# Optimization experiments

Hardware: AMD Instinct MI355X
Metric: run time of the kernel (lower is better)

Reference implementation:

```python
import jax, jax.numpy as jnp
import numpy as np

K = 7          # involution kernel size
GC = 16        # group_channels
BN_EPS = 1e-5


def conv1x1(x, w, b):
    # x: [b,c,h,w], w: [o,c], b: [o]
    return jnp.einsum('bchw,oc->bohw', x, w) + b[None, :, None, None]


def involution(x, w1, b1, w2, b2):
    # x: [b,c,h,w]; stride=1, kernel K, padding K//2
    b_, c, h, w = x.shape
    g = c // GC
    # per-pixel kernel weights: conv1x1 -> conv1x1 (no activation, as in source)
    wgt = conv1x1(conv1x1(x, w1, b1), w2, b2).reshape(b_, g, K * K, h, w)
    # patches: [b, c*K*K, h, w] with channel-major (c, kh, kw) ordering, matching torch Unfold
    pat = jax.lax.conv_general_dilated_patches(
        x, (K, K), (1, 1), ((K // 2, K // 2), (K // 2, K // 2)))
    pat = pat.reshape(b_, g, GC, K * K, h, w)
    out = jnp.einsum('bgkhw,bgckhw->bgchw', wgt, pat)
    return out.reshape(b_, c, h, w)


def hswish(x):
    return x * jnp.clip(x + 3.0, 0.0, 6.0) / 6.0


def setup_inputs() -> dict:
    key = jax.random.key(0)
    ks = jax.random.split(key, 20)
    inp, oup, mip = 256, 256, 64
    n, h, w = 16, 96, 96
    rr = 4  # involution reduction_ratio

    def rn(k, shape, s=0.05):
        return (jax.random.normal(k, shape) * s).astype(jnp.float32)

    def invp(k0, k1, k2, k3):
        return (rn(k0, (mip // rr, mip)), rn(k1, (mip // rr,)),
                rn(k2, (K * K * (mip // GC), mip // rr)),
                rn(k3, (K * K * (mip // GC),)))

    d = {}
    d['x'] = jax.random.normal(ks[0], (n, inp, h, w), dtype=jnp.float32)
    d['w_c1'] = rn(ks[1], (mip, inp)); d['b_c1'] = rn(ks[2], (mip,))
    d['inv1_w1'], d['inv1_b1'], d['inv1_w2'], d['inv1_b2'] = invp(ks[3], ks[4], ks[5], ks[6])
    d['bn_g'] = jnp.ones(mip, jnp.float32); d['bn_b'] = jnp.zeros(mip, jnp.float32)
    d['bn_m'] = jnp.zeros(mip, jnp.float32); d['bn_v'] = jnp.ones(mip, jnp.float32)
    d['invh_w1'], d['invh_b1'], d['invh_w2'], d['invh_b2'] = invp(ks[7], ks[8], ks[9], ks[10])
    d['w_h'] = rn(ks[11], (oup, mip)); d['b_h'] = rn(ks[12], (oup,))
    d['invw_w1'], d['invw_b1'], d['invw_w2'], d['invw_b2'] = invp(ks[13], ks[14], ks[15], ks[16])
    d['w_w'] = rn(ks[17], (oup, mip)); d['b_w'] = rn(ks[18], (oup,))
    return d


def reference(x, w_c1, b_c1, inv1_w1, inv1_b1, inv1_w2, inv1_b2,
              bn_g, bn_b, bn_m, bn_v,
              invh_w1, invh_b1, invh_w2, invh_b2, w_h, b_h,
              invw_w1, invw_b1, invw_w2, invw_b2, w_w, b_w):
    n, c, h, w = x.shape
    x_h = jnp.mean(x, axis=3, keepdims=True)                        # [n,c,h,1]
    x_w = jnp.mean(x, axis=2, keepdims=True).transpose(0, 1, 3, 2)  # [n,c,w,1]
    y = jnp.concatenate([x_h, x_w], axis=2)                          # [n,c,h+w,1]
    y = conv1x1(y, w_c1, b_c1)                                       # [n,mip,h+w,1]
    y = involution(y, inv1_w1, inv1_b1, inv1_w2, inv1_b2)
    inv_std = jax.lax.rsqrt(bn_v + BN_EPS)
    y = (y - bn_m[None, :, None, None]) * (bn_g * inv_std)[None, :, None, None] + bn_b[None, :, None, None]
    y = hswish(y)
    y_h = y[:, :, :h, :]                                             # [n,mip,h,1]
    y_w = y[:, :, h:, :].transpose(0, 1, 3, 2)                       # [n,mip,1,w]
    a_h = jax.nn.sigmoid(conv1x1(involution(y_h, invh_w1, invh_b1, invh_w2, invh_b2), w_h, b_h))
    a_w = jax.nn.sigmoid(conv1x1(involution(y_w, invw_w1, invw_b1, invw_w2, invw_b2), w_w, b_w))
    return x * a_w * a_h
```

## Files before the change

### kernel.cpp

```cpp
#include <hip/hip_runtime.h>
#include <math.h>

#define N_B   16
#define C_IN  256
#define MIP   64
#define HW    96
#define PTOT  192
#define KK    7

typedef float floatx4 __attribute__((ext_vector_type(4)));

__global__ void pool_kernel(const float* __restrict__ x, float* __restrict__ pooled) {
    int plane = blockIdx.x;
    const float* xp = x + (size_t)plane * (HW * HW);
    __shared__ float sm[HW * 97];
    int t = threadIdx.x;
    #pragma unroll
    for (int k = 0; k < 9; ++k) {
        int idx = t + k * 256;
        floatx4 v = ((const floatx4*)xp)[idx];
        int flat = idx * 4;
        int row = flat / HW;
        int col = flat - row * HW;
        float* d = &sm[row * 97 + col];
        d[0] = v.x; d[1] = v.y; d[2] = v.z; d[3] = v.w;
    }
    __syncthreads();
    float* pp = pooled + (size_t)plane * PTOT;
    if (t < HW) {
        float rs = 0.f;
        #pragma unroll 4
        for (int j = 0; j < HW; ++j) rs += sm[t * 97 + j];
        pp[t] = rs * (1.f / 96.f);
    } else if (t < 2 * HW) {
        int c = t - HW;
        float cs = 0.f;
        #pragma unroll 4
        for (int i = 0; i < HW; ++i) cs += sm[i * 97 + c];
        pp[HW + c] = cs * (1.f / 96.f);
    }
}

__global__ __launch_bounds__(256) void megamid_kernel(
    const float* __restrict__ pooled,
    const float* __restrict__ w_c1, const float* __restrict__ b_c1,
    const float* __restrict__ i1_w1, const float* __restrict__ i1_b1,
    const float* __restrict__ i1_w2, const float* __restrict__ i1_b2,
    const float* __restrict__ bn_g, const float* __restrict__ bn_b,
    const float* __restrict__ bn_m, const float* __restrict__ bn_v,
    const float* __restrict__ h_w1, const float* __restrict__ h_b1,
    const float* __restrict__ h_w2, const float* __restrict__ h_b2,
    const float* __restrict__ w_h,  const float* __restrict__ b_h,
    const float* __restrict__ v_w1, const float* __restrict__ v_b1,
    const float* __restrict__ v_w2, const float* __restrict__ v_b2,
    const float* __restrict__ w_w,  const float* __restrict__ b_w,
    float* __restrict__ a_h, float* __restrict__ a_w)
{
    int p0 = blockIdx.x * 16;
    int n  = blockIdx.y;
    int t  = threadIdx.x;
    int side = (p0 >= HW) ? 1 : 0;
    int lo = side * HW;

    __shared__ float smem[15552];
    float* pt   = smem;
    float* sw   = smem + 8192;
    float* y0t  = smem + 12352;
    float* yt   = smem + 14144;
    float* lt    = smem;
    float* lwgt  = smem + 352;
    float* lt2   = smem + 968;
    float* lwgt2 = smem + 1224;
    float* lz    = smem + 1672;

    const float* pn = pooled + (size_t)n * C_IN * PTOT;

    #pragma unroll
    for (int i = 0; i < 32; ++i) {
        int flat = t + 256 * i;
        int c = flat >> 5, j = flat & 31;
        int r = p0 - 6 + j;
        pt[flat] = (j < 28 && r >= 0 && r < PTOT) ? pn[c * PTOT + r] : 0.f;
    }

    int o = t & 63;
    int j0 = (t >> 6) * 8;
    float acc[8];
    #pragma unroll
    for (int e = 0; e < 8; ++e) acc[e] = 0.f;

    for (int c0 = 0; c0 < C_IN; c0 += 64) {
        __syncthreads();
        #pragma unroll
        for (int i = 0; i < 16; ++i) {
            int flat = t + 256 * i;
            int oo = flat >> 6, cc = flat & 63;
            sw[oo * 65 + cc] = w_c1[oo * C_IN + c0 + cc];
        }
        __syncthreads();
        #pragma unroll 4
        for (int cc = 0; cc < 64; ++cc) {
            float wv = sw[o * 65 + cc];
            const floatx4 pa = *(const floatx4*)&pt[(c0 + cc) * 32 + j0];
            const floatx4 pb = *(const floatx4*)&pt[(c0 + cc) * 32 + j0 + 4];
            acc[0] += wv * pa.x; acc[1] += wv * pa.y;
            acc[2] += wv * pa.z; acc[3] += wv * pa.w;
            acc[4] += wv * pb.x; acc[5] += wv * pb.y;
            acc[6] += wv * pb.z; acc[7] += wv * pb.w;
        }
    }
    {
        float bo = b_c1[o];
        #pragma unroll
        for (int e = 0; e < 8; ++e) {
            int j = j0 + e;
            if (j < 28) {
                int r = p0 - 6 + j;
                y0t[j * 64 + o] = (r >= 0 && r < PTOT) ? (acc[e] + bo) : 0.f;
            }
        }
    }
    __syncthreads();

    for (int idx = t; idx < 352; idx += 256) {
        int q = idx >> 4, i = idx & 15;
        float a = i1_b1[i];
        const float* wr = i1_w1 + i * MIP;
        #pragma unroll 8
        for (int oo = 0; oo < MIP; ++oo) a += wr[oo] * y0t[(q + 3) * 64 + oo];
        lt[idx] = a;
    }
    __syncthreads();
    for (int idx = t; idx < 616; idx += 256) {
        int q = idx / 28, m = idx - q * 28;
        int g = m / 7, ky = m - g * 7;
        int wq = g * 49 + ky * 7 + 3;
        float a = i1_b2[wq];
        const float* wr = i1_w2 + wq * 16;
        #pragma unroll
        for (int r = 0; r < 16; ++r) a += wr[r] * lt[q * 16 + r];
        lwgt[idx] = a;
    }
    __syncthreads();
    for (int idx = t; idx < 1408; idx += 256) {
        int q = idx >> 6, ch = idx & 63;
        int g = ch >> 4;
        float a = 0.f;
        #pragma unroll
        for (int ky = 0; ky < KK; ++ky)
            a += lwgt[q * 28 + g * 7 + ky] * y0t[(q + ky) * 64 + ch];
        float inv_std = rsqrtf(bn_v[ch] + 1e-5f);
        float v = (a - bn_m[ch]) * (bn_g[ch] * inv_std) + bn_b[ch];
        yt[idx] = v * fminf(fmaxf(v + 3.f, 0.f), 6.f) * (1.f / 6.f);
    }
    __syncthreads();

    const float* ww1 = side ? v_w1 : h_w1;
    const float* bb1 = side ? v_b1 : h_b1;
    const float* ww2 = side ? v_w2 : h_w2;
    const float* bb2 = side ? v_b2 : h_b2;
    const float* wf  = side ? w_w  : w_h;
    const float* bf  = side ? b_w  : b_h;

    {
        int pp = t >> 4, i = t & 15;
        float a = bb1[i];
        const float* wr = ww1 + i * MIP;
        #pragma unroll 8
        for (int oo = 0; oo < MIP; ++oo) a += wr[oo] * yt[(pp + 3) * 64 + oo];
        lt2[t] = a;
    }
    __syncthreads();
    for (int idx = t; idx < 448; idx += 256) {
        int pp = idx / 28, m = idx - pp * 28;
        int g = m / 7, kk = m - g * 7;
        int wq = side ? (g * 49 + 21 + kk) : (g * 49 + kk * 7 + 3);
        float a = bb2[wq];
        const float* wr = ww2 + wq * 16;
        #pragma unroll
        for (int r = 0; r < 16; ++r) a += wr[r] * lt2[pp * 16 + r];
        lwgt2[idx] = a;
    }
    __syncthreads();
    for (int idx = t; idx < 1024; idx += 256) {
        int pp = idx >> 6, ch = idx & 63;
        int g = ch >> 4;
        float a = 0.f;
        #pragma unroll
        for (int k = 0; k < KK; ++k) {
            int pos = p0 + pp + k - 3;
            float v = (pos >= lo && pos < lo + HW) ? yt[(pp + k) * 64 + ch] : 0.f;
            a += lwgt2[pp * 28 + g * 7 + k] * v;
        }
        lz[idx] = a;
    }
    __syncthreads();
    {
        int co = t;
        float accf[16];
        float bfv = bf[co];
        #pragma unroll
        for (int pp = 0; pp < 16; ++pp) accf[pp] = bfv;
        const float* wr = wf + co * MIP;
        for (int ch = 0; ch < MIP; ++ch) {
            float wv = wr[ch];
            #pragma unroll
            for (int pp = 0; pp < 16; ++pp)
                accf[pp] += wv * lz[pp * 64 + ch];
        }
        float* dst = side ? a_w : a_h;
        size_t basep = ((size_t)n * C_IN + co) * HW + (p0 - lo);
        #pragma unroll
        for (int pp = 0; pp < 16; ++pp)
            dst[basep + pp] = 1.f / (1.f + __expf(-accf[pp]));
    }
}

__global__ void apply_kernel(const float* __restrict__ x,
                             const float* __restrict__ a_h, const float* __restrict__ a_w,
                             float* __restrict__ out) {
    int plane = blockIdx.x;
    const floatx4* xp = (const floatx4*)(x + (size_t)plane * (HW * HW));
    floatx4* op = (floatx4*)(out + (size_t)plane * (HW * HW));
    __shared__ float sah[HW];
    __shared__ float saw[HW];
    int t = threadIdx.x;
    if (t < HW) {
        sah[t] = a_h[(size_t)plane * HW + t];
        saw[t] = a_w[(size_t)plane * HW + t];
    }
    __syncthreads();
    #pragma unroll
    for (int k = 0; k < 9; ++k) {
        int idx = t + k * 256;
        floatx4 v = xp[idx];
        int row = idx / 24;
        int c4 = (idx - row * 24) * 4;
        float ah = sah[row];
        v.x *= ah * saw[c4 + 0];
        v.y *= ah * saw[c4 + 1];
        v.z *= ah * saw[c4 + 2];
        v.w *= ah * saw[c4 + 3];
        __builtin_nontemporal_store(v, &op[idx]);
    }
}

extern "C" void kernel_launch(void* const* d_in, const int* in_sizes, int n_in,
                              void* d_out, int out_size, void* d_ws, size_t ws_size,
                              hipStream_t stream) {
    const float* x      = (const float*)d_in[0];
    const float* w_c1   = (const float*)d_in[1];
    const float* b_c1   = (const float*)d_in[2];
    const float* i1_w1  = (const float*)d_in[3];
    const float* i1_b1  = (const float*)d_in[4];
    const float* i1_w2  = (const float*)d_in[5];
    const float* i1_b2  = (const float*)d_in[6];
    const float* bn_g   = (const float*)d_in[7];
    const float* bn_b   = (const float*)d_in[8];
    const float* bn_m   = (const float*)d_in[9];
    const float* bn_v   = (const float*)d_in[10];
    const float* ih_w1  = (const float*)d_in[11];
    const float* ih_b1  = (const float*)d_in[12];
    const float* ih_w2  = (const float*)d_in[13];
    const float* ih_b2  = (const float*)d_in[14];
    const float* w_h    = (const float*)d_in[15];
    const float* b_h    = (const float*)d_in[16];
    const float* iw_w1  = (const float*)d_in[17];
    const float* iw_b1  = (const float*)d_in[18];
    const float* iw_w2  = (const float*)d_in[19];
    const float* iw_b2  = (const float*)d_in[20];
    const float* w_w    = (const float*)d_in[21];
    const float* b_w    = (const float*)d_in[22];
    float* out = (float*)d_out;

    float* ws = (float*)d_ws;
    float* pooled = ws;
    float* a_h    = pooled + 786432;
    float* a_w    = a_h + 393216;

    pool_kernel<<<dim3(N_B * C_IN), dim3(256), 0, stream>>>(x, pooled);
    megamid_kernel<<<dim3(12, N_B), dim3(256), 0, stream>>>(
        pooled, w_c1, b_c1, i1_w1, i1_b1, i1_w2, i1_b2,
        bn_g, bn_b, bn_m, bn_v,
        ih_w1, ih_b1, ih_w2, ih_b2, w_h, b_h,
        iw_w1, iw_b1, iw_w2, iw_b2, w_w, b_w, a_h, a_w);
    apply_kernel<<<dim3(N_B * C_IN), dim3(256), 0, stream>>>(x, a_h, a_w, out);
}
```

Baseline: 353.8 us.

## Split fused mid kernel into conv, involution and final projection kernels

Splits the monolithic per-block pipeline into three kernels: a 1x1 conv over pooled features, the involution/BN/hswish stage with smaller position tiles, and a final projection+sigmoid kernel with many more blocks. The intermediates go through global workspace buffers that alias earlier, already-consumed buffers. The aim is to replace a low-occupancy, 192-block kernel that ran long serial phases with higher parallelism. The cost is extra launches and global round trips for the intermediates.

```diff
diff --git a/kernel.cpp b/kernel.cpp
--- a/kernel.cpp
+++ b/kernel.cpp
@@ -41,97 +41,75 @@
     }
 }
 
-__global__ __launch_bounds__(256) void megamid_kernel(
+__global__ __launch_bounds__(256) void conv_kernel(
     const float* __restrict__ pooled,
     const float* __restrict__ w_c1, const float* __restrict__ b_c1,
+    float* __restrict__ y0g)
+{
+    int t = threadIdx.x;
+    int o  = t & 63;
+    int pl = t >> 6;
+    int p  = blockIdx.x * 4 + pl;
+    int n  = blockIdx.y;
+    const float* pr = pooled + (size_t)n * C_IN * PTOT + p;
+    const floatx4* wr = (const floatx4*)(w_c1 + o * C_IN);
+    float acc = 0.f;
+    #pragma unroll 8
+    for (int c4 = 0; c4 < C_IN / 4; ++c4) {
+        floatx4 w4 = wr[c4];
+        int c = c4 * 4;
+        acc += w4.x * pr[(c + 0) * PTOT];
+        acc += w4.y * pr[(c + 1) * PTOT];
+        acc += w4.z * pr[(c + 2) * PTOT];
+        acc += w4.w * pr[(c + 3) * PTOT];
+    }
+    y0g[((size_t)n * PTOT + p) * 64 + o] = acc + b_c1[o];
+}
+
+__global__ __launch_bounds__(256) void mid_kernel(
+    const float* __restrict__ y0g,
     const float* __restrict__ i1_w1, const float* __restrict__ i1_b1,
     const float* __restrict__ i1_w2, const float* __restrict__ i1_b2,
     const float* __restrict__ bn_g, const float* __restrict__ bn_b,
     const float* __restrict__ bn_m, const float* __restrict__ bn_v,
     const float* __restrict__ h_w1, const float* __restrict__ h_b1,
     const float* __restrict__ h_w2, const float* __restrict__ h_b2,
-    const float* __restrict__ w_h,  const float* __restrict__ b_h,
     const float* __restrict__ v_w1, const float* __restrict__ v_b1,
     const float* __restrict__ v_w2, const float* __restrict__ v_b2,
-    const float* __restrict__ w_w,  const float* __restrict__ b_w,
-    float* __restrict__ a_h, float* __restrict__ a_w)
+    float* __restrict__ lzg)
 {
-    int p0 = blockIdx.x * 16;
+    int p0 = blockIdx.x * 8;
     int n  = blockIdx.y;
     int t  = threadIdx.x;
     int side = (p0 >= HW) ? 1 : 0;
     int lo = side * HW;
 
-    __shared__ float smem[15552];
-    float* pt   = smem;
-    float* sw   = smem + 8192;
-    float* y0t  = smem + 12352;
-    float* yt   = smem + 14144;
-    float* lt    = smem;
-    float* lwgt  = smem + 352;
-    float* lt2   = smem + 968;
-    float* lwgt2 = smem + 1224;
-    float* lz    = smem + 1672;
-
-    const float* pn = pooled + (size_t)n * C_IN * PTOT;
+    __shared__ float y0t[20 * 64];
+    __shared__ float yt[14 * 64];
+    __shared__ float lt[14 * 16];
+    __shared__ float lwgt[14 * 28];
+    __shared__ float lt2[8 * 16];
+    __shared__ float lwgt2[8 * 28];
 
     #pragma unroll
-    for (int i = 0; i < 32; ++i) {
+    for (int i = 0; i < 5; ++i) {
         int flat = t + 256 * i;
-        int c = flat >> 5, j = flat & 31;
+        int j = flat >> 6, o = flat & 63;
         int r = p0 - 6 + j;
-        pt[flat] = (j < 28 && r >= 0 && r < PTOT) ? pn[c * PTOT + r] : 0.f;
-    }
-
-    int o = t & 63;
-    int j0 = (t >> 6) * 8;
-    float acc[8];
-    #pragma unroll
-    for (int e = 0; e < 8; ++e) acc[e] = 0.f;
-
-    for (int c0 = 0; c0 < C_IN; c0 += 64) {
-        __syncthreads();
-        #pragma unroll
-        for (int i = 0; i < 16; ++i) {
-            int flat = t + 256 * i;
-            int oo = flat >> 6, cc = flat & 63;
-            sw[oo * 65 + cc] = w_c1[oo * C_IN + c0 + cc];
-        }
-        __syncthreads();
-        #pragma unroll 4
-        for (int cc = 0; cc < 64; ++cc) {
-            float wv = sw[o * 65 + cc];
-            const floatx4 pa = *(const floatx4*)&pt[(c0 + cc) * 32 + j0];
-            const floatx4 pb = *(const floatx4*)&pt[(c0 + cc) * 32 + j0 + 4];
-            acc[0] += wv * pa.x; acc[1] += wv * pa.y;
-            acc[2] += wv * pa.z; acc[3] += wv * pa.w;
-            acc[4] += wv * pb.x; acc[5] += wv * pb.y;
-            acc[6] += wv * pb.z; acc[7] += wv * pb.w;
-        }
-    }
-    {
-        float bo = b_c1[o];
-        #pragma unroll
-        for (int e = 0; e < 8; ++e) {
-            int j = j0 + e;
-            if (j < 28) {
-                int r = p0 - 6 + j;
-                y0t[j * 64 + o] = (r >= 0 && r < PTOT) ? (acc[e] + bo) : 0.f;
-            }
-        }
-    }
-    __syncthreads();
-
-    for (int idx = t; idx < 352; idx += 256) {
-        int q = idx >> 4, i = idx & 15;
+        y0t[flat] = (r >= 0 && r < PTOT) ? y0g[((size_t)n * PTOT + r) * 64 + o] : 0.f;
+    }
+    __syncthreads();
+
+    if (t < 224) {
+        int q = t >> 4, i = t & 15;
         float a = i1_b1[i];
         const float* wr = i1_w1 + i * MIP;
         #pragma unroll 8
         for (int oo = 0; oo < MIP; ++oo) a += wr[oo] * y0t[(q + 3) * 64 + oo];
-        lt[idx] = a;
-    }
-    __syncthreads();
-    for (int idx = t; idx < 616; idx += 256) {
+        lt[t] = a;
+    }
+    __syncthreads();
+    for (int idx = t; idx < 392; idx += 256) {
         int q = idx / 28, m = idx - q * 28;
         int g = m / 7, ky = m - g * 7;
         int wq = g * 49 + ky * 7 + 3;
@@ -142,7 +120,7 @@
         lwgt[idx] = a;
     }
     __syncthreads();
-    for (int idx = t; idx < 1408; idx += 256) {
+    for (int idx = t; idx < 896; idx += 256) {
         int q = idx >> 6, ch = idx & 63;
         int g = ch >> 4;
         float a = 0.f;
@@ -159,10 +137,8 @@
     const float* bb1 = side ? v_b1 : h_b1;
     const float* ww2 = side ? v_w2 : h_w2;
     const float* bb2 = side ? v_b2 : h_b2;
-    const float* wf  = side ? w_w  : w_h;
-    const float* bf  = side ? b_w  : b_h;
-
-    {
+
+    if (t < 128) {
         int pp = t >> 4, i = t & 15;
         float a = bb1[i];
         const float* wr = ww1 + i * MIP;
@@ -171,18 +147,18 @@
         lt2[t] = a;
     }
     __syncthreads();
-    for (int idx = t; idx < 448; idx += 256) {
-        int pp = idx / 28, m = idx - pp * 28;
+    if (t < 224) {
+        int pp = t / 28, m = t - pp * 28;
         int g = m / 7, kk = m - g * 7;
         int wq = side ? (g * 49 + 21 + kk) : (g * 49 + kk * 7 + 3);
         float a = bb2[wq];
         const float* wr = ww2 + wq * 16;
         #pragma unroll
         for (int r = 0; r < 16; ++r) a += wr[r] * lt2[pp * 16 + r];
-        lwgt2[idx] = a;
-    }
-    __syncthreads();
-    for (int idx = t; idx < 1024; idx += 256) {
+        lwgt2[t] = a;
+    }
+    __syncthreads();
+    for (int idx = t; idx < 512; idx += 256) {
         int pp = idx >> 6, ch = idx & 63;
         int g = ch >> 4;
         float a = 0.f;
@@ -192,28 +168,37 @@
             float v = (pos >= lo && pos < lo + HW) ? yt[(pp + k) * 64 + ch] : 0.f;
             a += lwgt2[pp * 28 + g * 7 + k] * v;
         }
-        lz[idx] = a;
-    }
-    __syncthreads();
-    {
-        int co = t;
-        float accf[16];
-        float bfv = bf[co];
-        #pragma unroll
-        for (int pp = 0; pp < 16; ++pp) accf[pp] = bfv;
-        const float* wr = wf + co * MIP;
-        for (int ch = 0; ch < MIP; ++ch) {
-            float wv = wr[ch];
-            #pragma unroll
-            for (int pp = 0; pp < 16; ++pp)
-                accf[pp] += wv * lz[pp * 64 + ch];
-        }
-        float* dst = side ? a_w : a_h;
-        size_t basep = ((size_t)n * C_IN + co) * HW + (p0 - lo);
-        #pragma unroll
-        for (int pp = 0; pp < 16; ++pp)
-            dst[basep + pp] = 1.f / (1.f + __expf(-accf[pp]));
-    }
+        lzg[((size_t)n * PTOT + p0 + pp) * 64 + ch] = a;
+    }
+}
+
+__global__ __launch_bounds__(384) void final_kernel(
+    const float* __restrict__ lzg,
+    const float* __restrict__ w_h, const float* __restrict__ b_h,
+    const float* __restrict__ w_w, const float* __restrict__ b_w,
+    float* __restrict__ a_h, float* __restrict__ a_w)
+{
+    int side = blockIdx.z;
+    int n    = blockIdx.y;
+    int co0  = blockIdx.x * 4;
+    int t    = threadIdx.x;
+    int lo   = side * HW;
+    __shared__ float lzs[HW * 65];
+    const float* src = lzg + ((size_t)n * PTOT + lo) * 64;
+    for (int flat = t; flat < HW * 64; flat += 384) {
+        int pp = flat >> 6, ch = flat & 63;
+        lzs[pp * 65 + ch] = src[flat];
+    }
+    __syncthreads();
+    int p_l  = t % HW;
+    int co_l = t / HW;
+    int co   = co0 + co_l;
+    const float* wr = (side ? w_w : w_h) + co * MIP;
+    float acc = (side ? b_w : b_h)[co];
+    #pragma unroll 8
+    for (int ch = 0; ch < MIP; ++ch) acc += wr[ch] * lzs[p_l * 65 + ch];
+    float* dst = side ? a_w : a_h;
+    dst[((size_t)n * C_IN + co) * HW + p_l] = 1.f / (1.f + __expf(-acc));
 }
 
 __global__ void apply_kernel(const float* __restrict__ x,
@@ -277,12 +262,17 @@
     float* pooled = ws;
     float* a_h    = pooled + 786432;
     float* a_w    = a_h + 393216;
+    float* lzg    = pooled;
+    float* y0g    = a_h;
 
     pool_kernel<<<dim3(N_B * C_IN), dim3(256), 0, stream>>>(x, pooled);
-    megamid_kernel<<<dim3(12, N_B), dim3(256), 0, stream>>>(
-        pooled, w_c1, b_c1, i1_w1, i1_b1, i1_w2, i1_b2,
+    conv_kernel<<<dim3(48, N_B), dim3(256), 0, stream>>>(pooled, w_c1, b_c1, y0g);
+    mid_kernel<<<dim3(24, N_B), dim3(256), 0, stream>>>(
+        y0g, i1_w1, i1_b1, i1_w2, i1_b2,
         bn_g, bn_b, bn_m, bn_v,
-        ih_w1, ih_b1, ih_w2, ih_b2, w_h, b_h,
-        iw_w1, iw_b1, iw_w2, iw_b2, w_w, b_w, a_h, a_w);
+        ih_w1, ih_b1, ih_w2, ih_b2,
+        iw_w1, iw_b1, iw_w2, iw_b2, lzg);
+    final_kernel<<<dim3(64, N_B, 2), dim3(384), 0, stream>>>(
+        lzg, w_h, b_h, w_w, b_w, a_h, a_w);
     apply_kernel<<<dim3(N_B * C_IN), dim3(256), 0, stream>>>(x, a_h, a_w, out);
 }
```

Result: slower. 369.8 us (+4.5%).
